# Kernel tuning notes

Measured on AMD Instinct MI355X. Metric: run time of the kernel, lower is better.

## Reference

```python
import jax, jax.numpy as jnp
import numpy as np

N_PATCHES = 256
PATCH = 16
D = 768
H = 12
DH = D // H
L = 12
OUT_D = 10
EPS = 1e-5


def _pos_embed(seq_len, d):
    i = np.arange(seq_len)[:, None].astype(np.float64)
    j = np.arange(d)[None, :].astype(np.float64)
    angle_even = i / 10000 ** (j / d)
    angle_odd = i / 10000 ** ((j - 1) / d)
    pe = np.where(np.arange(d)[None, :] % 2 == 0, np.sin(angle_even), np.cos(angle_odd))
    return jnp.asarray(pe, dtype=jnp.float32)


def _layernorm(x, g, b):
    mu = jnp.mean(x, axis=-1, keepdims=True)
    var = jnp.var(x, axis=-1, keepdims=True)
    return (x - mu) * jax.lax.rsqrt(var + EPS) * g + b


def setup_inputs() -> dict:
    key = jax.random.key(0)
    ks = jax.random.split(key, 16)
    s = 0.02
    return {
        "images": jax.random.normal(ks[0], (64, 1, N_PATCHES * PATCH), dtype=jnp.float32),
        "Wemb": jax.random.normal(ks[1], (D, PATCH), dtype=jnp.float32) * s,
        "bemb": jnp.zeros((D,), jnp.float32),
        "cls": jax.random.uniform(ks[2], (1, D), dtype=jnp.float32),
        "Wq": jax.random.normal(ks[3], (L, H, DH, DH), dtype=jnp.float32) * s,
        "bq": jnp.zeros((L, H, DH), jnp.float32),
        "Wk": jax.random.normal(ks[4], (L, H, DH, DH), dtype=jnp.float32) * s,
        "bk": jnp.zeros((L, H, DH), jnp.float32),
        "Wv": jax.random.normal(ks[5], (L, H, DH, DH), dtype=jnp.float32) * s,
        "bv": jnp.zeros((L, H, DH), jnp.float32),
        "ln1_g": jnp.ones((L, D), jnp.float32),
        "ln1_b": jnp.zeros((L, D), jnp.float32),
        "ln2_g": jnp.ones((L, D), jnp.float32),
        "ln2_b": jnp.zeros((L, D), jnp.float32),
        "W1": jax.random.normal(ks[6], (L, 4 * D, D), dtype=jnp.float32) * s,
        "b1": jnp.zeros((L, 4 * D), jnp.float32),
        "W2": jax.random.normal(ks[7], (L, D, 4 * D), dtype=jnp.float32) * s,
        "b2": jnp.zeros((L, D), jnp.float32),
        "Whead": jax.random.normal(ks[8], (OUT_D, D), dtype=jnp.float32) * s,
        "bhead": jnp.zeros((OUT_D,), jnp.float32),
    }


def reference(images, Wemb, bemb, cls, Wq, bq, Wk, bk, Wv, bv,
              ln1_g, ln1_b, ln2_g, ln2_b, W1, b1, W2, b2, Whead, bhead):
    n = images.shape[0]
    # patchify: (N,1,Lspec) -> (N, n_patches, patch_size)
    patches = images.reshape(n, N_PATCHES, PATCH)
    tok = jnp.einsum("npi,di->npd", patches, Wemb) + bemb  # linear embed
    tok = jnp.concatenate([jnp.broadcast_to(cls[None], (n, 1, D)), tok], axis=1)
    tok = tok + _pos_embed(N_PATCHES + 1, D)[None]  # (N, S, D), S = 257

    scale = 1.0 / jnp.sqrt(jnp.float32(DH))
    for l in range(L):
        x = tok
        h = _layernorm(x, ln1_g[l], ln1_b[l]).reshape(n, -1, H, DH)
        q = jnp.einsum("nshd,hod->nsho", h, Wq[l]) + bq[l][None, None]
        k = jnp.einsum("nshd,hod->nsho", h, Wk[l]) + bk[l][None, None]
        v = jnp.einsum("nshd,hod->nsho", h, Wv[l]) + bv[l][None, None]
        att = jax.nn.softmax(jnp.einsum("nqho,nkho->nhqk", q, k) * scale, axis=-1)
        o = jnp.einsum("nhqk,nkho->nqho", att, v).reshape(n, -1, D)
        x = x + o  # residual (no output projection in original MSA)
        h2 = _layernorm(x, ln2_g[l], ln2_b[l])
        mlp = jax.nn.gelu(jnp.einsum("nsd,fd->nsf", h2, W1[l]) + b1[l], approximate=False)
        tok = x + jnp.einsum("nsf,df->nsd", mlp, W2[l]) + b2[l]

    logits = tok[:, 0] @ Whead.T + bhead
    return jax.nn.softmax(logits, axis=-1)
```

## Files before the change

kernel.cpp:

```cpp
#include <hip/hip_runtime.h>
#include <math.h>
#include <stdint.h>

#define N_IMG 64
#define S_LEN 257
#define D_MODEL 768
#define H_HEADS 12
#define L_LAYERS 12
#define F_HID 3072
#define OUT_DIM 10
#define R_ROWS (N_IMG * S_LEN)
#define R_PAD 16512
#define SKV 320

typedef unsigned short ushort_t;
typedef __attribute__((ext_vector_type(4))) float f32x4;
typedef __attribute__((ext_vector_type(8))) short short8;
typedef __attribute__((ext_vector_type(2))) unsigned int u32x2;

__device__ __forceinline__ ushort_t f2bf(float x) {
    unsigned u = __float_as_uint(x);
    u += 0x7fffu + ((u >> 16) & 1u);
    return (ushort_t)(u >> 16);
}
__device__ __forceinline__ unsigned pack2(float a, float b) {
    return (unsigned)f2bf(a) | ((unsigned)f2bf(b) << 16);
}

__device__ __forceinline__ void glds16(const ushort_t* g, const ushort_t* l) {
    __builtin_amdgcn_global_load_lds(
        (const __attribute__((address_space(1))) unsigned int*)(uintptr_t)g,
        (__attribute__((address_space(3))) unsigned int*)(uintptr_t)l,
        16, 0, 0);
}

__global__ __launch_bounds__(256) void pos_kernel(float* __restrict__ pos) {
    int i = blockIdx.x;
    int t = threadIdx.x;
    for (int u = 0; u < 3; ++u) {
        int j = t + 256 * u;
        double e = (double)(j & ~1) / 768.0;
        double angle = (double)i * exp(-e * 9.210340371976184);
        double v = (j & 1) ? cos(angle) : sin(angle);
        pos[i * 768 + j] = (float)v;
    }
}

__global__ __launch_bounds__(256) void embed_kernel(const float* __restrict__ images,
                                                    const float* __restrict__ Wemb,
                                                    const float* __restrict__ bemb,
                                                    const float* __restrict__ cls,
                                                    const float* __restrict__ pos,
                                                    float* __restrict__ tok) {
    int b = blockIdx.x;
    int n = b / S_LEN, s = b % S_LEN;
    int t = threadIdx.x;
    __shared__ float p[16];
    if (s > 0 && t < 16) p[t] = images[n * 4096 + (s - 1) * 16 + t];
    __syncthreads();
    for (int u = 0; u < 3; ++u) {
        int d = t + 256 * u;
        float acc;
        if (s == 0) {
            acc = cls[d];
        } else {
            acc = bemb[d];
            const float4* w = (const float4*)(Wemb + d * 16);
            float4 w0 = w[0], w1 = w[1], w2 = w[2], w3 = w[3];
            acc += p[0] * w0.x + p[1] * w0.y + p[2] * w0.z + p[3] * w0.w;
            acc += p[4] * w1.x + p[5] * w1.y + p[6] * w1.z + p[7] * w1.w;
            acc += p[8] * w2.x + p[9] * w2.y + p[10] * w2.z + p[11] * w2.w;
            acc += p[12] * w3.x + p[13] * w3.y + p[14] * w3.z + p[15] * w3.w;
        }
        tok[(size_t)b * 768 + d] = acc + pos[s * 768 + d];
    }
}

__global__ __launch_bounds__(256) void ln_kernel(const float* __restrict__ x,
                                                 const float* __restrict__ g,
                                                 const float* __restrict__ b,
                                                 ushort_t* __restrict__ y) {
    int row = blockIdx.x * 4 + (threadIdx.x >> 6);
    int lane = threadIdx.x & 63;
    const float* xr = x + (size_t)row * 768 + lane * 4;
    float4 a0 = *(const float4*)xr;
    float4 a1 = *(const float4*)(xr + 256);
    float4 a2 = *(const float4*)(xr + 512);
    float s = (a0.x + a0.y + a0.z + a0.w) + (a1.x + a1.y + a1.z + a1.w) + (a2.x + a2.y + a2.z + a2.w);
    float sq = a0.x*a0.x + a0.y*a0.y + a0.z*a0.z + a0.w*a0.w
             + a1.x*a1.x + a1.y*a1.y + a1.z*a1.z + a1.w*a1.w
             + a2.x*a2.x + a2.y*a2.y + a2.z*a2.z + a2.w*a2.w;
    for (int o = 32; o; o >>= 1) {
        s += __shfl_xor(s, o);
        sq += __shfl_xor(sq, o);
    }
    float mu = s * (1.0f / 768.0f);
    float var = sq * (1.0f / 768.0f) - mu * mu;
    float rs = rsqrtf(var + 1e-5f);
    ushort_t* yr = y + (size_t)row * 768 + lane * 4;
#pragma unroll
    for (int i = 0; i < 3; ++i) {
        float4 av = (i == 0) ? a0 : (i == 1) ? a1 : a2;
        const float4 gg = *(const float4*)(g + lane * 4 + i * 256);
        const float4 bb = *(const float4*)(b + lane * 4 + i * 256);
        float o0 = (av.x - mu) * rs * gg.x + bb.x;
        float o1 = (av.y - mu) * rs * gg.y + bb.y;
        float o2 = (av.z - mu) * rs * gg.z + bb.z;
        float o3 = (av.w - mu) * rs * gg.w + bb.w;
        *(u32x2*)(yr + i * 256) = (u32x2){pack2(o0, o1), pack2(o2, o3)};
    }
}

__global__ __launch_bounds__(256) void conv_layer(const float* __restrict__ Wq,
                                                  const float* __restrict__ Wk,
                                                  const float* __restrict__ Wv,
                                                  const float* __restrict__ W1l,
                                                  const float* __restrict__ W2l,
                                                  ushort_t* __restrict__ wqkvbf,
                                                  ushort_t* __restrict__ w1bf,
                                                  ushort_t* __restrict__ w2bf) {
    const int NQKV = H_HEADS * 192 * 64;
    const int NW = F_HID * D_MODEL;
    int idx = (blockIdx.x * 256 + threadIdx.x) * 4;
    if (idx < NQKV) {
        int h = idx / (192 * 64);
        int rem = idx - h * 192 * 64;
        int o3 = rem >> 6, d = rem & 63;
        const float* src;
        int o;
        if (o3 < 64)       { src = Wq; o = o3; }
        else if (o3 < 128) { src = Wk; o = o3 - 64; }
        else               { src = Wv; o = o3 - 128; }
        float4 v = *(const float4*)(src + ((size_t)(h * 64 + o)) * 64 + d);
        *(u32x2*)(wqkvbf + idx) = (u32x2){pack2(v.x, v.y), pack2(v.z, v.w)};
    } else if (idx < NQKV + NW) {
        int i = idx - NQKV;
        float4 v = *(const float4*)(W1l + i);
        *(u32x2*)(w1bf + i) = (u32x2){pack2(v.x, v.y), pack2(v.z, v.w)};
    } else {
        int i = idx - NQKV - NW;
        float4 v = *(const float4*)(W2l + i);
        *(u32x2*)(w2bf + i) = (u32x2){pack2(v.x, v.y), pack2(v.z, v.w)};
    }
}

__global__ __launch_bounds__(256) void qkv_mfma(const ushort_t* __restrict__ xbf,
                                                const ushort_t* __restrict__ wqkv,
                                                const float* __restrict__ bq,
                                                const float* __restrict__ bk,
                                                const float* __restrict__ bv,
                                                ushort_t* __restrict__ qhb,
                                                ushort_t* __restrict__ khb,
                                                ushort_t* __restrict__ vtb) {
    __shared__ ushort_t As[128 * 64];
    int rt = blockIdx.x;
    int h = blockIdx.y;
    int t = threadIdx.x, lane = t & 63, wid = t >> 6;
    int wr = wid >> 1, wc = wid & 1;
    {
        int lr = t >> 3, lg = t & 7;
#pragma unroll
        for (int u = 0; u < 4; ++u) {
            int r = u * 32 + lr;
            int grow = rt * 128 + r;
            if (grow >= R_ROWS) grow = R_ROWS - 1;
            short8 a = *(const short8*)(xbf + (size_t)grow * 768 + h * 64 + lg * 8);
            *(short8*)&As[r * 64 + (lg ^ (r & 7)) * 8] = a;
        }
    }
    __syncthreads();
    int frow = lane & 15, g = lane >> 4;
    const ushort_t* wb = wqkv + (size_t)h * (192 * 64);
    f32x4 acc[4][6];
#pragma unroll
    for (int m = 0; m < 4; ++m)
#pragma unroll
        for (int n = 0; n < 6; ++n) acc[m][n] = (f32x4){0.f, 0.f, 0.f, 0.f};
#pragma unroll
    for (int kk = 0; kk < 2; ++kk) {
        short8 af[4], bfr[6];
#pragma unroll
        for (int m = 0; m < 4; ++m) {
            int r = wr * 64 + m * 16 + frow;
            af[m] = *(const short8*)&As[r * 64 + ((kk * 4 + g) ^ (r & 7)) * 8];
        }
#pragma unroll
        for (int n = 0; n < 6; ++n)
            bfr[n] = *(const short8*)(wb + (size_t)(wc * 96 + n * 16 + frow) * 64 + kk * 32 + g * 8);
#pragma unroll
        for (int m = 0; m < 4; ++m)
#pragma unroll
            for (int n = 0; n < 6; ++n)
                acc[m][n] = __builtin_amdgcn_mfma_f32_16x16x32_bf16(bfr[n], af[m], acc[m][n], 0, 0, 0);
    }
#pragma unroll
    for (int m = 0; m < 4; ++m) {
        int token = rt * 128 + wr * 64 + m * 16 + frow;
        if (token < R_ROWS) {
            unsigned nimg = (unsigned)token / 257u;
            unsigned s = (unsigned)token - nimg * 257u;
            size_t qk_base = ((size_t)(nimg * H_HEADS + h) * 257 + s) * 64;
            size_t v_base = (size_t)(nimg * H_HEADS + h) * (64 * SKV);
#pragma unroll
            for (int n = 0; n < 6; ++n) {
                int c = wc * 96 + n * 16 + g * 4;
                f32x4 a = acc[m][n];
                if (c < 64) {
                    const float4 bb = *(const float4*)(bq + h * 64 + c);
                    *(u32x2*)(qhb + qk_base + c) = (u32x2){
                        pack2((a[0] + bb.x) * 0.125f, (a[1] + bb.y) * 0.125f),
                        pack2((a[2] + bb.z) * 0.125f, (a[3] + bb.w) * 0.125f)};
                } else if (c < 128) {
                    const float4 bb = *(const float4*)(bk + h * 64 + (c - 64));
                    *(u32x2*)(khb + qk_base + (c - 64)) = (u32x2){
                        pack2(a[0] + bb.x, a[1] + bb.y), pack2(a[2] + bb.z, a[3] + bb.w)};
                } else {
                    const float4 bb = *(const float4*)(bv + h * 64 + (c - 128));
                    vtb[v_base + (size_t)(c - 128 + 0) * SKV + s] = f2bf(a[0] + bb.x);
                    vtb[v_base + (size_t)(c - 128 + 1) * SKV + s] = f2bf(a[1] + bb.y);
                    vtb[v_base + (size_t)(c - 128 + 2) * SKV + s] = f2bf(a[2] + bb.z);
                    vtb[v_base + (size_t)(c - 128 + 3) * SKV + s] = f2bf(a[3] + bb.w);
                }
            }
        }
    }
}

template <int NST>
__global__ __launch_bounds__(256) void attn_mfma(const ushort_t* __restrict__ qh,
                                                 const ushort_t* __restrict__ kh,
                                                 const ushort_t* __restrict__ vT,
                                                 float* __restrict__ tok) {
    __shared__ ushort_t Plds[4][NST][1024];
    int b = blockIdx.x;
    int nh, base;
    if (NST == 2) { nh = b % 768; base = (b / 768) * 128; }
    else          { nh = b;       base = 256; }
    int h = nh % H_HEADS, n = nh / H_HEADS;
    int t = threadIdx.x, w = t >> 6, lane = t & 63;
    int lq = lane & 15, g = lane >> 4;
    const size_t hoff = ((size_t)n * H_HEADS + h) * (S_LEN * 64);
    const ushort_t* qhp = qh + hoff;
    const ushort_t* khp = kh + hoff;
    const ushort_t* vp  = vT + ((size_t)n * H_HEADS + h) * (64 * SKV);
    const int xorm = (lq & 7) << 4;

    short8 qf[NST][2];
    int qr0[NST];
    float m[NST], lsum[NST];
    f32x4 o[NST][4];
#pragma unroll
    for (int s = 0; s < NST; ++s) {
        int qrow = base + s * 64 + w * 16 + lq;
        qr0[s] = qrow;
        int qcl = qrow > 256 ? 256 : qrow;
#pragma unroll
        for (int kk = 0; kk < 2; ++kk)
            qf[s][kk] = *(const short8*)(qhp + (size_t)qcl * 64 + kk * 32 + g * 8);
        m[s] = -INFINITY; lsum[s] = 0.f;
#pragma unroll
        for (int dt = 0; dt < 4; ++dt) o[s][dt] = (f32x4){0.f, 0.f, 0.f, 0.f};
    }

    for (int kt = 0; kt < 5; ++kt) {
        short8 ah[4][2];
#pragma unroll
        for (int st = 0; st < 4; ++st) {
            int key = kt * 64 + st * 16 + lq;
            int kcl = key > 256 ? 256 : key;
            const ushort_t* krh = khp + (size_t)kcl * 64 + g * 8;
            ah[st][0] = *(const short8*)krh;
            ah[st][1] = *(const short8*)(krh + 32);
        }
        f32x4 c[NST][4];
#pragma unroll
        for (int s = 0; s < NST; ++s)
#pragma unroll
            for (int st = 0; st < 4; ++st) {
                c[s][st] = (f32x4){0.f, 0.f, 0.f, 0.f};
#pragma unroll
                for (int kk = 0; kk < 2; ++kk)
                    c[s][st] = __builtin_amdgcn_mfma_f32_16x16x32_bf16(ah[st][kk], qf[s][kk], c[s][st], 0, 0, 0);
            }
        float scale[NST];
        unsigned pw[NST][4][2];
#pragma unroll
        for (int s = 0; s < NST; ++s) {
            float tmax = -INFINITY;
#pragma unroll
            for (int st = 0; st < 4; ++st)
#pragma unroll
                for (int j = 0; j < 4; ++j) {
                    int key = kt * 64 + st * 16 + g * 4 + j;
                    float sv = (key <= 256) ? c[s][st][j] : -INFINITY;
                    c[s][st][j] = sv;
                    tmax = fmaxf(tmax, sv);
                }
            tmax = fmaxf(tmax, __shfl_xor(tmax, 16));
            tmax = fmaxf(tmax, __shfl_xor(tmax, 32));
            float mn = fmaxf(m[s], tmax);
            scale[s] = __expf(m[s] - mn);
            float psum = 0.f;
#pragma unroll
            for (int st = 0; st < 4; ++st) {
                float p0 = __expf(c[s][st][0] - mn), p1 = __expf(c[s][st][1] - mn);
                float p2 = __expf(c[s][st][2] - mn), p3 = __expf(c[s][st][3] - mn);
                psum += (p0 + p1) + (p2 + p3);
                pw[s][st][0] = pack2(p0, p1);
                pw[s][st][1] = pack2(p2, p3);
            }
            psum += __shfl_xor(psum, 16);
            psum += __shfl_xor(psum, 32);
            lsum[s] = lsum[s] * scale[s] + psum;
            m[s] = mn;
        }
#pragma unroll
        for (int s = 0; s < NST; ++s) {
            char* pwave = (char*)&Plds[w][s][0];
#pragma unroll
            for (int st = 0; st < 4; ++st) {
                int off = (lq * 128 + st * 32 + g * 8) ^ xorm;
                *(u32x2*)(pwave + off) = (u32x2){pw[s][st][0], pw[s][st][1]};
            }
#pragma unroll
            for (int dt = 0; dt < 4; ++dt) {
                o[s][dt][0] *= scale[s]; o[s][dt][1] *= scale[s];
                o[s][dt][2] *= scale[s]; o[s][dt][3] *= scale[s];
            }
        }
#pragma unroll
        for (int kk = 0; kk < 2; ++kk) {
            short8 pf[NST];
#pragma unroll
            for (int s = 0; s < NST; ++s) {
                int roff = (lq * 128 + kk * 64 + g * 16) ^ xorm;
                pf[s] = *(const short8*)((char*)&Plds[w][s][0] + roff);
            }
#pragma unroll
            for (int dt = 0; dt < 4; ++dt) {
                short8 vf = *(const short8*)(vp + (size_t)(dt * 16 + lq) * SKV + kt * 64 + kk * 32 + g * 8);
#pragma unroll
                for (int s = 0; s < NST; ++s)
                    o[s][dt] = __builtin_amdgcn_mfma_f32_16x16x32_bf16(vf, pf[s], o[s][dt], 0, 0, 0);
            }
        }
    }
#pragma unroll
    for (int s = 0; s < NST; ++s) {
        if (qr0[s] < S_LEN) {
            float inv = 1.0f / lsum[s];
            float* trow = tok + ((size_t)n * S_LEN + qr0[s]) * 768 + h * 64 + g * 4;
#pragma unroll
            for (int dt = 0; dt < 4; ++dt) {
                float4 old = *(const float4*)(trow + dt * 16);
                old.x += o[s][dt][0] * inv;
                old.y += o[s][dt][1] * inv;
                old.z += o[s][dt][2] * inv;
                old.w += o[s][dt][3] * inv;
                *(float4*)(trow + dt * 16) = old;
            }
        }
    }
}

__device__ __forceinline__ float gelu_fast(float x) {
    float s = fabsf(x) * 0.70710678118654752f;
    float t = 1.0f / (1.0f + 0.3275911f * s);
    float y = t * (0.254829592f + t * (-0.284496736f + t * (1.421413741f +
              t * (-1.453152027f + t * 1.061405429f))));
    float erfa = 1.0f - y * __expf(-s * s);
    float erfv = copysignf(erfa, x);
    return 0.5f * x * (1.0f + erfv);
}

template <int MODE>
__global__ __launch_bounds__(256) void mfma_gemm(const ushort_t* __restrict__ A,
                                                 const ushort_t* __restrict__ B,
                                                 const float* __restrict__ bias,
                                                 void* __restrict__ Cv,
                                                 int K, int lda, int ldb, int ldc) {
    __shared__ ushort_t As[2][128 * 64];
    __shared__ ushort_t Bs[2][128 * 64];
    int t = threadIdx.x;
    int lane = t & 63, wid = t >> 6;
    int wr = wid >> 1, wc = wid & 1;
    int bm = blockIdx.y, bn = blockIdx.x;
    const ushort_t* Ag = A + (size_t)(bm * 128) * lda;
    const ushort_t* Bg = B + (size_t)(bn * 128) * ldb;
    int srow = t >> 3;
    int swz = ((t & 7) ^ (srow & 7)) * 8;
    int wbase = (t & 192) * 8;
    int frow = lane & 15, g = lane >> 4;
    f32x4 acc[4][4];
#pragma unroll
    for (int m = 0; m < 4; ++m)
#pragma unroll
        for (int n = 0; n < 4; ++n) acc[m][n] = (f32x4){0.f, 0.f, 0.f, 0.f};

    auto STAGE = [&](int buf, int k0) {
#pragma unroll
        for (int u = 0; u < 4; ++u) {
            glds16(Ag + (size_t)(u * 32 + srow) * lda + k0 + swz, &As[buf][u * 2048 + wbase]);
            glds16(Bg + (size_t)(u * 32 + srow) * ldb + k0 + swz, &Bs[buf][u * 2048 + wbase]);
        }
    };
    STAGE(0, 0);
    asm volatile("s_waitcnt vmcnt(0)" ::: "memory");
    __builtin_amdgcn_s_barrier();
    int nt = K >> 6;
    int cur = 0;
    for (int it = 0; it < nt; ++it) {
        if (it + 1 < nt) STAGE(cur ^ 1, (it + 1) * 64);
        const ushort_t* Ab = &As[cur][0];
        const ushort_t* Bb = &Bs[cur][0];
#pragma unroll
        for (int kk = 0; kk < 2; ++kk) {
            short8 af[4], bfr[4];
#pragma unroll
            for (int mi = 0; mi < 4; ++mi) {
                int r = wr * 64 + mi * 16 + frow;
                af[mi] = *(const short8*)&Ab[r * 64 + ((kk * 4 + g) ^ (r & 7)) * 8];
            }
#pragma unroll
            for (int ni = 0; ni < 4; ++ni) {
                int r = wc * 64 + ni * 16 + frow;
                bfr[ni] = *(const short8*)&Bb[r * 64 + ((kk * 4 + g) ^ (r & 7)) * 8];
            }
#pragma unroll
            for (int mi = 0; mi < 4; ++mi)
#pragma unroll
                for (int ni = 0; ni < 4; ++ni)
                    acc[mi][ni] = __builtin_amdgcn_mfma_f32_16x16x32_bf16(bfr[ni], af[mi], acc[mi][ni], 0, 0, 0);
        }
        if (it + 1 < nt) {
            asm volatile("s_waitcnt vmcnt(0) lgkmcnt(0)" ::: "memory");
            __builtin_amdgcn_s_barrier();
            cur ^= 1;
        }
    }
    int row0 = bm * 128 + wr * 64 + frow;
    int col0 = bn * 128 + wc * 64 + g * 4;
#pragma unroll
    for (int n = 0; n < 4; ++n) {
        int col = col0 + n * 16;
        float4 bb = {0.f, 0.f, 0.f, 0.f};
        if (bias) bb = *(const float4*)(bias + col);
#pragma unroll
        for (int mi = 0; mi < 4; ++mi) {
            int row = row0 + mi * 16;
            f32x4 a = acc[mi][n];
            float v0 = a[0] + bb.x, v1 = a[1] + bb.y, v2 = a[2] + bb.z, v3 = a[3] + bb.w;
            if (MODE == 0) {
                v0 = gelu_fast(v0); v1 = gelu_fast(v1); v2 = gelu_fast(v2); v3 = gelu_fast(v3);
                *(u32x2*)((ushort_t*)Cv + (size_t)row * ldc + col) =
                    (u32x2){pack2(v0, v1), pack2(v2, v3)};
            } else {
                float* cp = (float*)Cv + (size_t)row * ldc + col;
                float4 old = *(const float4*)cp;
                old.x += v0; old.y += v1; old.z += v2; old.w += v3;
                *(float4*)cp = old;
            }
        }
    }
}

__global__ __launch_bounds__(64) void head_kernel(const float* __restrict__ tok,
                                                  const float* __restrict__ Whead,
                                                  const float* __restrict__ bhead,
                                                  float* __restrict__ out) {
    int n = blockIdx.x;
    int t = threadIdx.x;
    __shared__ float logits[OUT_DIM];
    if (t < OUT_DIM) {
        float acc = bhead[t];
        const float* xr = tok + (size_t)n * S_LEN * 768;
        const float* w = Whead + t * 768;
        for (int d = 0; d < 768; ++d) acc += xr[d] * w[d];
        logits[t] = acc;
    }
    __syncthreads();
    if (t == 0) {
        float m = -INFINITY;
        for (int o = 0; o < OUT_DIM; ++o) m = fmaxf(m, logits[o]);
        float ssum = 0.f;
        float e[OUT_DIM];
        for (int o = 0; o < OUT_DIM; ++o) { e[o] = expf(logits[o] - m); ssum += e[o]; }
        float inv = 1.0f / ssum;
        for (int o = 0; o < OUT_DIM; ++o) out[n * OUT_DIM + o] = e[o] * inv;
    }
}

extern "C" void kernel_launch(void* const* d_in, const int* in_sizes, int n_in,
                              void* d_out, int out_size, void* d_ws, size_t ws_size,
                              hipStream_t stream) {
    const float* images = (const float*)d_in[0];
    const float* Wemb   = (const float*)d_in[1];
    const float* bemb   = (const float*)d_in[2];
    const float* cls    = (const float*)d_in[3];
    const float* Wq     = (const float*)d_in[4];
    const float* bq     = (const float*)d_in[5];
    const float* Wk     = (const float*)d_in[6];
    const float* bk     = (const float*)d_in[7];
    const float* Wv     = (const float*)d_in[8];
    const float* bv     = (const float*)d_in[9];
    const float* ln1_g  = (const float*)d_in[10];
    const float* ln1_b  = (const float*)d_in[11];
    const float* ln2_g  = (const float*)d_in[12];
    const float* ln2_b  = (const float*)d_in[13];
    const float* W1     = (const float*)d_in[14];
    const float* b1     = (const float*)d_in[15];
    const float* W2     = (const float*)d_in[16];
    const float* b2     = (const float*)d_in[17];
    const float* Whead  = (const float*)d_in[18];
    const float* bhead  = (const float*)d_in[19];
    float* out = (float*)d_out;

    const size_t TOKP = (size_t)R_PAD * D_MODEL;
    const size_t QKSZ = (size_t)N_IMG * H_HEADS * S_LEN * 64;
    const size_t VTSZ = (size_t)N_IMG * H_HEADS * 64 * SKV;
    const size_t WSZ  = (size_t)F_HID * D_MODEL;
    float* ws   = (float*)d_ws;
    float* pos  = ws;
    float* tok  = pos + 197376;
    ushort_t* xbf  = (ushort_t*)(tok + TOKP);
    ushort_t* qhb  = xbf + TOKP;
    ushort_t* khb  = qhb + QKSZ;
    ushort_t* vtb  = khb + QKSZ;
    ushort_t* wqkvbf = vtb + VTSZ;
    ushort_t* w1bf = wqkvbf + H_HEADS * 192 * 64;
    ushort_t* w2bf = w1bf + WSZ;
    ushort_t* hid_full = w2bf + WSZ;

    const size_t hid_bytes = (size_t)R_PAD * F_HID * 2;
    const size_t needed = ((char*)hid_full - (char*)d_ws) + hid_bytes;
    int nchunk = (ws_size >= needed) ? 1 : 2;
    int FC = F_HID / nchunk;
    ushort_t* hid = (nchunk == 1) ? hid_full : qhb;

    pos_kernel<<<S_LEN, 256, 0, stream>>>(pos);
    embed_kernel<<<R_ROWS, 256, 0, stream>>>(images, Wemb, bemb, cls, pos, tok);

    for (int l = 0; l < L_LAYERS; ++l) {
        const size_t wqkv_off = (size_t)l * H_HEADS * 64 * 64;
        const size_t bqkv_off = (size_t)l * H_HEADS * 64;
        ln_kernel<<<R_ROWS / 4, 256, 0, stream>>>(tok, ln1_g + l * 768, ln1_b + l * 768, xbf);
        conv_layer<<<4752, 256, 0, stream>>>(
            Wq + wqkv_off, Wk + wqkv_off, Wv + wqkv_off,
            W1 + (size_t)l * WSZ, W2 + (size_t)l * WSZ,
            wqkvbf, w1bf, w2bf);
        qkv_mfma<<<dim3(R_PAD / 128, H_HEADS), 256, 0, stream>>>(
            xbf, wqkvbf, bq + bqkv_off, bk + bqkv_off, bv + bqkv_off, qhb, khb, vtb);
        attn_mfma<2><<<N_IMG * H_HEADS * 2, 256, 0, stream>>>(qhb, khb, vtb, tok);
        attn_mfma<1><<<N_IMG * H_HEADS, 256, 0, stream>>>(qhb, khb, vtb, tok);
        ln_kernel<<<R_ROWS / 4, 256, 0, stream>>>(tok, ln2_g + l * 768, ln2_b + l * 768, xbf);
        for (int c = 0; c < nchunk; ++c) {
            int c0 = c * FC;
            mfma_gemm<0><<<dim3(FC / 128, R_PAD / 128), 256, 0, stream>>>(
                xbf, w1bf + (size_t)c0 * D_MODEL, b1 + (size_t)l * F_HID + c0, hid,
                768, 768, 768, FC);
            mfma_gemm<1><<<dim3(D_MODEL / 128, R_PAD / 128), 256, 0, stream>>>(
                hid, w2bf + c0, (c == 0) ? (b2 + (size_t)l * D_MODEL) : (const float*)nullptr,
                tok, FC, FC, F_HID, D_MODEL);
        }
    }
    head_kernel<<<N_IMG, 64, 0, stream>>>(tok, Whead, bhead, out);
}
```

Before: 4.999 ms.

## Remap GEMM blocks per XCD for L2 reuse and rebalance attention query splits

```diff
diff --git a/kernel.cpp b/kernel.cpp
--- a/kernel.cpp
+++ b/kernel.cpp
@@ -230,12 +230,9 @@
 __global__ __launch_bounds__(256) void attn_mfma(const ushort_t* __restrict__ qh,
                                                  const ushort_t* __restrict__ kh,
                                                  const ushort_t* __restrict__ vT,
-                                                 float* __restrict__ tok) {
+                                                 float* __restrict__ tok, int base) {
     __shared__ ushort_t Plds[4][NST][1024];
-    int b = blockIdx.x;
-    int nh, base;
-    if (NST == 2) { nh = b % 768; base = (b / 768) * 128; }
-    else          { nh = b;       base = 256; }
+    int nh = blockIdx.x;
     int h = nh % H_HEADS, n = nh / H_HEADS;
     int t = threadIdx.x, w = t >> 6, lane = t & 63;
     int lq = lane & 15, g = lane >> 4;
@@ -378,17 +375,24 @@
                                                  const ushort_t* __restrict__ B,
                                                  const float* __restrict__ bias,
                                                  void* __restrict__ Cv,
-                                                 int K, int lda, int ldb, int ldc) {
+                                                 int K, int lda, int ldb, int ldc, int nbn) {
     __shared__ ushort_t As[2][128 * 64];
     __shared__ ushort_t Bs[2][128 * 64];
+    int nwg = gridDim.x;
+    int orig = blockIdx.x;
+    int xcd = orig & 7, idx = orig >> 3;
+    int q8 = nwg >> 3, r8 = nwg & 7;
+    int cbase = (xcd < r8) ? xcd * (q8 + 1) : r8 * (q8 + 1) + (xcd - r8) * q8;
+    int swz = cbase + idx;
+    int bm = swz / nbn, bn = swz - bm * nbn;
+
     int t = threadIdx.x;
     int lane = t & 63, wid = t >> 6;
     int wr = wid >> 1, wc = wid & 1;
-    int bm = blockIdx.y, bn = blockIdx.x;
     const ushort_t* Ag = A + (size_t)(bm * 128) * lda;
     const ushort_t* Bg = B + (size_t)(bn * 128) * ldb;
     int srow = t >> 3;
-    int swz = ((t & 7) ^ (srow & 7)) * 8;
+    int swzo = ((t & 7) ^ (srow & 7)) * 8;
     int wbase = (t & 192) * 8;
     int frow = lane & 15, g = lane >> 4;
     f32x4 acc[4][4];
@@ -400,8 +404,8 @@
     auto STAGE = [&](int buf, int k0) {
 #pragma unroll
         for (int u = 0; u < 4; ++u) {
-            glds16(Ag + (size_t)(u * 32 + srow) * lda + k0 + swz, &As[buf][u * 2048 + wbase]);
-            glds16(Bg + (size_t)(u * 32 + srow) * ldb + k0 + swz, &Bs[buf][u * 2048 + wbase]);
+            glds16(Ag + (size_t)(u * 32 + srow) * lda + k0 + swzo, &As[buf][u * 2048 + wbase]);
+            glds16(Bg + (size_t)(u * 32 + srow) * ldb + k0 + swzo, &Bs[buf][u * 2048 + wbase]);
         }
     };
     STAGE(0, 0);
@@ -550,17 +554,17 @@
             wqkvbf, w1bf, w2bf);
         qkv_mfma<<<dim3(R_PAD / 128, H_HEADS), 256, 0, stream>>>(
             xbf, wqkvbf, bq + bqkv_off, bk + bqkv_off, bv + bqkv_off, qhb, khb, vtb);
-        attn_mfma<2><<<N_IMG * H_HEADS * 2, 256, 0, stream>>>(qhb, khb, vtb, tok);
-        attn_mfma<1><<<N_IMG * H_HEADS, 256, 0, stream>>>(qhb, khb, vtb, tok);
+        attn_mfma<2><<<N_IMG * H_HEADS, 256, 0, stream>>>(qhb, khb, vtb, tok, 0);
+        attn_mfma<3><<<N_IMG * H_HEADS, 256, 0, stream>>>(qhb, khb, vtb, tok, 128);
         ln_kernel<<<R_ROWS / 4, 256, 0, stream>>>(tok, ln2_g + l * 768, ln2_b + l * 768, xbf);
         for (int c = 0; c < nchunk; ++c) {
             int c0 = c * FC;
-            mfma_gemm<0><<<dim3(FC / 128, R_PAD / 128), 256, 0, stream>>>(
+            mfma_gemm<0><<<(FC / 128) * (R_PAD / 128), 256, 0, stream>>>(
                 xbf, w1bf + (size_t)c0 * D_MODEL, b1 + (size_t)l * F_HID + c0, hid,
-                768, 768, 768, FC);
-            mfma_gemm<1><<<dim3(D_MODEL / 128, R_PAD / 128), 256, 0, stream>>>(
+                768, 768, 768, FC, FC / 128);
+            mfma_gemm<1><<<(D_MODEL / 128) * (R_PAD / 128), 256, 0, stream>>>(
                 hid, w2bf + c0, (c == 0) ? (b2 + (size_t)l * D_MODEL) : (const float*)nullptr,
-                tok, FC, FC, F_HID, D_MODEL);
+                tok, FC, FC, F_HID, D_MODEL, D_MODEL / 128);
         }
     }
     head_kernel<<<N_IMG, 64, 0, stream>>>(tok, Whead, bhead, out);
```

After: 4.823 ms. 1.04x faster.
